# Kernel optimization log

Hardware: AMD Instinct MI355X
Metric: run time of the kernel (lower is better)

Reference implementation:

```python
import jax, jax.numpy as jnp
from jax import lax
import numpy as np

B, T, C = 4, 2048, 1024
H = 4                      # num_heads
D = C // H                 # head_dim
EPS_N = 1e-6               # normalizer eps in scan
EPS_GN = 1e-5              # GroupNorm eps (torch default)


def setup_inputs() -> dict:
    key = jax.random.key(0)
    ks = jax.random.split(key, 8)
    s = 0.02
    return {
        "x": jax.random.normal(ks[0], (B, T, C), jnp.float32),
        "conv_w": jax.random.normal(ks[1], (C, 1, 4), jnp.float32) * s,
        "conv_b": jax.random.normal(ks[2], (C,), jnp.float32) * s,
        "wx_w": jax.random.normal(ks[3], (4 * C, C), jnp.float32) * s,
        "wx_b": jax.random.normal(ks[4], (4 * C,), jnp.float32) * s,
        "gn_w": jnp.ones((C,), jnp.float32),
        "gn_b": jnp.zeros((C,), jnp.float32),
        "out_w": jax.random.normal(ks[5], (C, C), jnp.float32) * s,
        "out_b": jax.random.normal(ks[6], (C,), jnp.float32) * s,
    }


def _slstm_scan(i_g, f_g, z_g, o_g):
    # all inputs (B,T,H,D); scan over time
    def step(carry, g):
        c, n, m = carry
        i_t, f_t, z_t, o_t = g
        m_t = jnp.maximum(f_t + m, i_t)
        i_p = jnp.exp(i_t - m_t)
        f_p = jnp.exp(f_t + m - m_t)
        c_t = f_p * c + i_p * z_t
        n_t = f_p * n + i_p
        h_t = jax.nn.sigmoid(o_t) * (c_t / (n_t + EPS_N))
        return (c_t, n_t, m_t), h_t

    tfirst = lambda a: jnp.transpose(a, (1, 0, 2, 3))  # (T,B,H,D)
    init = (jnp.zeros((B, H, D), i_g.dtype),
            jnp.ones((B, H, D), i_g.dtype),
            jnp.zeros((B, H, D), i_g.dtype))
    _, h_seq = lax.scan(step, init, (tfirst(i_g), tfirst(f_g), tfirst(z_g), tfirst(o_g)))
    return jnp.transpose(h_seq, (1, 0, 2, 3))  # (B,T,H,D)


def reference(x, conv_w, conv_b, wx_w, wx_b, gn_w, gn_b, out_w, out_b):
    # causal depthwise conv (torch pad=3 both sides, sliced to first T == left pad 3)
    xc = jnp.transpose(x, (0, 2, 1))  # (B,C,T)
    xc = lax.conv_general_dilated(
        xc, conv_w, window_strides=(1,), padding=[(3, 0)],
        dimension_numbers=("NCH", "OIH", "NCH"), feature_group_count=C)
    xc = jax.nn.silu(xc + conv_b[None, :, None])
    xc = jnp.transpose(xc, (0, 2, 1))  # (B,T,C)

    gates = jnp.einsum("btc,gc->btg", xc, wx_w) + wx_b  # (B,T,4C)
    gates = gates.reshape(B, T, 4, H, D)
    i_g, f_g, z_g, o_g = (gates[:, :, k] for k in range(4))
    z_g = jnp.tanh(z_g)

    h = _slstm_scan(i_g, f_g, z_g, o_g).reshape(B, T, C)

    # GroupNorm(H groups) over (B,C,T): normalize per (batch, group) over (D, T)
    hg = h.reshape(B, T, H, D)
    mean = hg.mean(axis=(1, 3), keepdims=True)
    var = hg.var(axis=(1, 3), keepdims=True)
    hn = ((hg - mean) / jnp.sqrt(var + EPS_GN)).reshape(B, T, C)
    hn = hn * gn_w + gn_b

    out = jnp.einsum("btc,oc->bto", hn, out_w) + out_b
    return out + x  # dropout is identity at inference
```

## Files before the change

### kernel.cpp

```cpp
#include <hip/hip_runtime.h>

#define B_ 4
#define T_ 2048
#define C_ 1024
#define H_ 4
#define D_ 256
#define M_ (B_*T_)
#define N1_ (4*C_)
#define K_ C_
#define LANES_ (B_*C_)
#define CHUNK_ 32
#define NCHUNK_ (T_/CHUNK_)

typedef unsigned short u16;
typedef unsigned int u32;
typedef __bf16 bf16x8 __attribute__((ext_vector_type(8)));
typedef float f32x4 __attribute__((ext_vector_type(4)));
typedef float vf4 __attribute__((ext_vector_type(4)));
typedef unsigned short u16x4 __attribute__((ext_vector_type(4)));
typedef unsigned short u16x8 __attribute__((ext_vector_type(8)));

__device__ __forceinline__ u16 f2bf(float f) {
  union { float f; u32 u; } v; v.f = f;
  u32 u = v.u;
  u32 r = (u + 0x7FFFu + ((u >> 16) & 1u)) >> 16;
  return (u16)r;
}
__device__ __forceinline__ float b2f(u16 h) {
  union { u32 u; float f; } v; v.u = ((u32)h) << 16;
  return v.f;
}

#define NCAST_ ((N1_*K_ + C_*C_) / 2048)

__global__ void prep_kernel(const float* __restrict__ wx_w, const float* __restrict__ out_w,
                            u16* __restrict__ w1p, u16* __restrict__ w2,
                            const float* __restrict__ x, const float* __restrict__ cw,
                            const float* __restrict__ cb, u16* __restrict__ xc,
                            float* __restrict__ stats) {
  if (blockIdx.x < NCAST_) {
    int i8 = (blockIdx.x * 256 + threadIdx.x) * 8;
    u16x8 o;
    if (i8 < N1_ * K_) {
      int n = i8 >> 10, k8 = i8 & 1023;
      const float* src = wx_w + (size_t)(((n & 3) << 10) | (n >> 2)) * K_ + k8;
      vf4 a = *(const vf4*)src;
      vf4 b = *(const vf4*)(src + 4);
#pragma unroll
      for (int j = 0; j < 4; ++j) { o[j] = f2bf(a[j]); o[j + 4] = f2bf(b[j]); }
      *(u16x8*)(w1p + i8) = o;
    } else {
      int j8 = i8 - N1_ * K_;
      vf4 a = *(const vf4*)(out_w + j8);
      vf4 b = *(const vf4*)(out_w + j8 + 4);
#pragma unroll
      for (int j = 0; j < 4; ++j) { o[j] = f2bf(a[j]); o[j + 4] = f2bf(b[j]); }
      *(u16x8*)(w2 + j8) = o;
    }
    return;
  }
  if (blockIdx.x == NCAST_ && threadIdx.x < 32) stats[threadIdx.x] = 0.f;
  int i4 = ((blockIdx.x - NCAST_) * 256 + threadIdx.x) * 4;
  int c = i4 & (C_ - 1);
  int t = (i4 >> 10) & (T_ - 1);
  vf4 acc = *(const vf4*)(cb + c);
  vf4 w0 = *(const vf4*)(cw + (size_t)c * 4);
  vf4 w1 = *(const vf4*)(cw + (size_t)(c + 1) * 4);
  vf4 w2v = *(const vf4*)(cw + (size_t)(c + 2) * 4);
  vf4 w3 = *(const vf4*)(cw + (size_t)(c + 3) * 4);
#pragma unroll
  for (int k = 0; k < 4; ++k) {
    if (t - 3 + k >= 0) {
      vf4 xv = *(const vf4*)(x + (size_t)i4 + (size_t)(k - 3) * C_);
      acc[0] = fmaf(w0[k], xv[0], acc[0]);
      acc[1] = fmaf(w1[k], xv[1], acc[1]);
      acc[2] = fmaf(w2v[k], xv[2], acc[2]);
      acc[3] = fmaf(w3[k], xv[3], acc[3]);
    }
  }
  u16x4 o;
#pragma unroll
  for (int j = 0; j < 4; ++j) {
    float s = acc[j] / (1.f + __expf(-acc[j]));
    o[j] = f2bf(s);
  }
  *(u16x4*)(xc + i4) = o;
}

template <int EPI>
__global__ __launch_bounds__(256, 3)
void gemm_bt(const u16* __restrict__ A, const u16* __restrict__ Bw,
             const float* __restrict__ bias, const float* __restrict__ resid,
             u16* __restrict__ obf, float* __restrict__ of32,
             f32x4* __restrict__ sSum, int M, int N, int K)
{
  __shared__ __align__(16) u16 smem[128 * 136];
  u16* a_s = smem;
  u16* b_s = smem + 128 * 64;

  const int tid  = threadIdx.x;
  const int lane = tid & 63;
  const int l15  = lane & 15;
  const int q    = lane >> 4;
  const int wave = tid >> 6;
  const int wm   = (wave >> 1) * 64;
  const int wn   = (wave & 1) * 64;
  const int bm   = blockIdx.y * 128;
  const int bn   = blockIdx.x * 128;

  const int srow   = wave * 8 + (lane >> 3);
  const int schunk = lane & 7;

  float bias4[4];
#pragma unroll
  for (int sn = 0; sn < 4; ++sn) {
    int gcol = bn + wn + sn * 16 + l15;
    bias4[sn] = (EPI == 0) ? bias[((gcol & 3) << 10) | (gcol >> 2)] : bias[gcol];
  }
  const bool zlane = (EPI == 0) && ((l15 & 3) == 2);

  f32x4 acc[4][4];
#pragma unroll
  for (int i = 0; i < 4; ++i)
#pragma unroll
    for (int j = 0; j < 4; ++j) acc[i][j] = (f32x4){0.f, 0.f, 0.f, 0.f};

  for (int k0 = 0; k0 < K; k0 += 64) {
#pragma unroll
    for (int i = 0; i < 4; ++i) {
      int r = i * 32 + srow;
      int lc = schunk ^ (r & 7);
      const u16* ga = A  + (size_t)(bm + r) * K + k0 + lc * 8;
      const u16* gb = Bw + (size_t)(bn + r) * K + k0 + lc * 8;
      __builtin_amdgcn_global_load_lds(
          (const __attribute__((address_space(1))) u32*)ga,
          (__attribute__((address_space(3))) u32*)&a_s[(i * 32 + wave * 8) * 64],
          16, 0, 0);
      __builtin_amdgcn_global_load_lds(
          (const __attribute__((address_space(1))) u32*)gb,
          (__attribute__((address_space(3))) u32*)&b_s[(i * 32 + wave * 8) * 64],
          16, 0, 0);
    }
    __syncthreads();
#pragma unroll
    for (int kk = 0; kk < 64; kk += 32) {
      const int kc = kk >> 3;
      bf16x8 af[4], bfr[4];
#pragma unroll
      for (int s = 0; s < 4; ++s) {
        int ra = wm + s * 16 + l15;
        int ph = (kc + q) ^ (ra & 7);
        af[s] = *(const bf16x8*)&a_s[ra * 64 + ph * 8];
      }
#pragma unroll
      for (int s = 0; s < 4; ++s) {
        int rb = wn + s * 16 + l15;
        int ph = (kc + q) ^ (rb & 7);
        bfr[s] = *(const bf16x8*)&b_s[rb * 64 + ph * 8];
      }
#pragma unroll
      for (int sm = 0; sm < 4; ++sm)
#pragma unroll
        for (int sn = 0; sn < 4; ++sn)
          acc[sm][sn] = __builtin_amdgcn_mfma_f32_16x16x32_bf16(af[sm], bfr[sn], acc[sm][sn], 0, 0, 0);
    }
    __syncthreads();
  }

  if (EPI == 0) {
#pragma unroll
    for (int smi = 0; smi < 4; ++smi) {
#pragma unroll
      for (int r = 0; r < 4; ++r) {
        int lrow = wm + smi * 16 + q * 4 + r;
#pragma unroll
        for (int sni = 0; sni < 4; ++sni) {
          int lcol = wn + sni * 16 + l15;
          float v = acc[smi][sni][r] + bias4[sni];
          if (zlane) {
            float e = __expf(2.f * v);
            v = (e - 1.f) / (e + 1.f);
          }
          smem[lrow * 136 + lcol] = f2bf(v);
        }
      }
    }
    __syncthreads();
#pragma unroll
    for (int it = 0; it < 8; ++it) {
      int flat = it * 256 + tid;
      int row = flat >> 4;
      int ch  = flat & 15;
      u16x8 vv = *(const u16x8*)&smem[row * 136 + ch * 8];
      *(u16x8*)(obf + (size_t)(bm + row) * N + bn + ch * 8) = vv;
    }
    if (tid < 128) {
      int ch = tid & 31, ck = tid >> 5;
      const u16* sp = smem + (ck * 32) * 136 + ch * 4;
      float F = 0.f, Mx = -1e30f, aBc = 0.f, aBn = 0.f;
#pragma unroll 8
      for (int t = 0; t < CHUNK_; ++t) {
        u16x4 gv = *(const u16x4*)(sp + t * 136);
        float i_t = b2f(gv[0]), f_t = b2f(gv[1]), z_t = b2f(gv[2]);
        float Mf = Mx + f_t;
        float Mn = fmaxf(Mf, i_t);
        float ea = __expf(Mf - Mn), eb = __expf(i_t - Mn);
        aBc = ea * aBc + eb * z_t;
        aBn = ea * aBn + eb;
        F += f_t; Mx = Mn;
      }
      int b = bm >> 11;
      int s = ((bm & 2047) >> 5) + ck;
      int cg = (bn >> 2) + ch;
      sSum[(size_t)s * LANES_ + b * C_ + cg] = (f32x4){F, Mx, aBc, aBn};
    }
  } else {
    float* fs = (float*)smem;
#pragma unroll
    for (int h = 0; h < 2; ++h) {
      __syncthreads();
#pragma unroll
      for (int smi2 = 0; smi2 < 2; ++smi2) {
        int smi = 2 * h + smi2;
#pragma unroll
        for (int r = 0; r < 4; ++r) {
          int slot = (wm >> 1) + smi2 * 16 + q * 4 + r;
#pragma unroll
          for (int sni = 0; sni < 4; ++sni) {
            int lcol = wn + sni * 16 + l15;
            fs[slot * 132 + lcol] = acc[smi][sni][r] + bias4[sni];
          }
        }
      }
      __syncthreads();
#pragma unroll
      for (int it = 0; it < 8; ++it) {
        int flat = it * 256 + tid;
        int slot = flat >> 5;
        int c4 = (flat & 31) * 4;
        int absrow = bm + ((slot & 32) << 1) + (h << 5) + (slot & 31);
        vf4 v = *(const vf4*)&fs[slot * 132 + c4];
        vf4 rv = *(const vf4*)(resid + (size_t)absrow * N + bn + c4);
        v[0] += rv[0]; v[1] += rv[1]; v[2] += rv[2]; v[3] += rv[3];
        *(vf4*)(of32 + (size_t)absrow * N + bn + c4) = v;
      }
    }
  }
}

__global__ void scan_prefix(const f32x4* __restrict__ sSum, f32x4* __restrict__ iSt) {
  int l = blockIdx.x * 256 + threadIdx.x;
  float ct = 0.f, nt = 1.f, mt = 0.f;
#pragma unroll 8
  for (int s = 0; s < NCHUNK_; ++s) {
    int idx = s * LANES_ + l;
    f32x4 S = sSum[idx];
    iSt[idx] = (f32x4){ct, nt, mt, 0.f};
    float mf = mt + S[0];
    float mn = fmaxf(mf, S[1]);
    float a = __expf(mf - mn);
    float bcoef = __expf(S[1] - mn);
    ct = a * ct + bcoef * S[2];
    nt = a * nt + bcoef * S[3];
    mt = mn;
  }
}

__global__ void scan_passB(const u16* __restrict__ gates, const f32x4* __restrict__ iSt,
                           u16* __restrict__ h, float* __restrict__ stats) {
  int tid = blockIdx.x * 256 + threadIdx.x;
  int lp = tid & 2047;
  int s = tid >> 11;
  int b = lp >> 9;
  int c2 = (lp & 511) * 2;
  const u16* g = gates + ((size_t)(b * T_ + s * CHUNK_) * C_ + c2) * 4;
  u16* hp = h + (size_t)(b * T_ + s * CHUNK_) * C_ + c2;
  int idx = s * LANES_ + b * C_ + c2;
  f32x4 S0 = iSt[idx], S1 = iSt[idx + 1];
  float cc0 = S0[0], nn0 = S0[1], mm0 = S0[2];
  float cc1 = S1[0], nn1 = S1[1], mm1 = S1[2];
  float ls = 0.f, lq = 0.f;
#pragma unroll 4
  for (int t = 0; t < CHUNK_; ++t) {
    u16x8 gv = *(const u16x8*)(g + (size_t)t * C_ * 4);
    float h0, h1;
    {
      float i_t = b2f(gv[0]), f_t = b2f(gv[1]), z_t = b2f(gv[2]), o_t = b2f(gv[3]);
      float m_new = fmaxf(f_t + mm0, i_t);
      float i_p = __expf(i_t - m_new);
      float f_p = __expf(f_t + mm0 - m_new);
      cc0 = f_p * cc0 + i_p * z_t;
      nn0 = f_p * nn0 + i_p;
      mm0 = m_new;
      float sig_o = 1.f / (1.f + __expf(-o_t));
      h0 = sig_o * (cc0 / (nn0 + 1e-6f));
    }
    {
      float i_t = b2f(gv[4]), f_t = b2f(gv[5]), z_t = b2f(gv[6]), o_t = b2f(gv[7]);
      float m_new = fmaxf(f_t + mm1, i_t);
      float i_p = __expf(i_t - m_new);
      float f_p = __expf(f_t + mm1 - m_new);
      cc1 = f_p * cc1 + i_p * z_t;
      nn1 = f_p * nn1 + i_p;
      mm1 = m_new;
      float sig_o = 1.f / (1.f + __expf(-o_t));
      h1 = sig_o * (cc1 / (nn1 + 1e-6f));
    }
    u16 hb0 = f2bf(h0), hb1 = f2bf(h1);
    float v0 = b2f(hb0), v1 = b2f(hb1);
    ls += v0 + v1; lq += v0 * v0 + v1 * v1;
    *(u32*)(hp + (size_t)t * C_) = (u32)hb0 | ((u32)hb1 << 16);
  }
  __shared__ float rs[256], rq[256];
  int thr = threadIdx.x;
  rs[thr] = ls; rq[thr] = lq;
  __syncthreads();
  for (int off = 64; off > 0; off >>= 1) {
    if ((thr & 127) < off) { rs[thr] += rs[thr + off]; rq[thr] += rq[thr + off]; }
    __syncthreads();
  }
  if ((thr & 127) == 0) {
    int grp = b * 4 + (c2 >> 8);
    atomicAdd(&stats[grp * 2 + 0], rs[thr]);
    atomicAdd(&stats[grp * 2 + 1], rq[thr]);
  }
}

__global__ void norm_kernel(const u16* __restrict__ h, const float* __restrict__ stats,
                            const float* __restrict__ gn_w, const float* __restrict__ gn_b,
                            u16* __restrict__ hn) {
  int i8 = (blockIdx.x * 256 + threadIdx.x) * 8;
  int c = i8 & (C_ - 1);
  int b = i8 >> 21;
  int grp = b * 4 + (c >> 8);
  const float inv_n = 1.f / (float)(T_ * D_);
  float mean = stats[grp * 2 + 0] * inv_n;
  float var  = stats[grp * 2 + 1] * inv_n - mean * mean;
  float rstd = rsqrtf(var + 1e-5f);
  u16x8 hv = *(const u16x8*)(h + i8);
  vf4 w0 = *(const vf4*)(gn_w + c), w1 = *(const vf4*)(gn_w + c + 4);
  vf4 b0 = *(const vf4*)(gn_b + c), b1 = *(const vf4*)(gn_b + c + 4);
  u16x8 o;
#pragma unroll
  for (int j = 0; j < 4; ++j) {
    o[j]     = f2bf((b2f(hv[j])     - mean) * rstd * w0[j] + b0[j]);
    o[j + 4] = f2bf((b2f(hv[j + 4]) - mean) * rstd * w1[j] + b1[j]);
  }
  *(u16x8*)(hn + i8) = o;
}

extern "C" void kernel_launch(void* const* d_in, const int* in_sizes, int n_in,
                              void* d_out, int out_size, void* d_ws, size_t ws_size,
                              hipStream_t stream) {
  const float* x      = (const float*)d_in[0];
  const float* conv_w = (const float*)d_in[1];
  const float* conv_b = (const float*)d_in[2];
  const float* wx_w   = (const float*)d_in[3];
  const float* wx_b   = (const float*)d_in[4];
  const float* gn_w   = (const float*)d_in[5];
  const float* gn_b   = (const float*)d_in[6];
  const float* out_w  = (const float*)d_in[7];
  const float* out_b  = (const float*)d_in[8];
  float* out = (float*)d_out;

  char* p = (char*)d_ws;
  u16* xc    = (u16*)p; p += (size_t)M_ * K_ * 2;
  u16* w1    = (u16*)p; p += (size_t)N1_ * K_ * 2;
  u16* w2    = (u16*)p; p += (size_t)C_ * C_ * 2;
  u16* gts   = (u16*)p; p += (size_t)M_ * N1_ * 2;
  u16* hb    = (u16*)p; p += (size_t)M_ * C_ * 2;
  u16* hn    = (u16*)p; p += (size_t)M_ * C_ * 2;
  float* stats = (float*)p; p += 256;
  const int nsum = LANES_ * NCHUNK_;
  f32x4* sSum = (f32x4*)p; p += (size_t)nsum * 16;
  f32x4* iSt  = (f32x4*)p; p += (size_t)nsum * 16;

  prep_kernel<<<NCAST_ + (M_ * C_) / 1024, 256, 0, stream>>>(
      wx_w, out_w, w1, w2, x, conv_w, conv_b, xc, stats);

  gemm_bt<0><<<dim3(N1_ / 128, M_ / 128), 256, 0, stream>>>(
      xc, w1, wx_b, nullptr, gts, nullptr, sSum, M_, N1_, K_);

  scan_prefix<<<LANES_ / 256, 256, 0, stream>>>(sSum, iSt);
  scan_passB<<<(2048 * NCHUNK_) / 256, 256, 0, stream>>>(gts, iSt, hb, stats);

  norm_kernel<<<(M_ * C_) / 2048, 256, 0, stream>>>(hb, stats, gn_w, gn_b, hn);

  gemm_bt<1><<<dim3(C_ / 128, M_ / 128), 256, 0, stream>>>(
      hn, w2, out_b, x, nullptr, out, nullptr, M_, C_, K_);
}
```

Baseline: 273.9 us.

## Fuse scan prefix, chunk scan and GroupNorm into one kernel with grid flags

Merges the prefix scan, per-chunk scan and normalization into a single persistent kernel that synchronizes via global atomic flags, keeping h values in registers instead of writing and re-reading an intermediate buffer. Also splits the GEMM epilogue chunk summary across all 256 threads with a two-segment combine. This removes two launches and a full intermediate round-trip but relies on all 512 blocks being co-resident for the spin barrier, and adds register pressure.

```diff
diff --git a/kernel.cpp b/kernel.cpp
--- a/kernel.cpp
+++ b/kernel.cpp
@@ -37,7 +37,7 @@
                             u16* __restrict__ w1p, u16* __restrict__ w2,
                             const float* __restrict__ x, const float* __restrict__ cw,
                             const float* __restrict__ cb, u16* __restrict__ xc,
-                            float* __restrict__ stats) {
+                            float* __restrict__ stats, int* __restrict__ flags) {
   if (blockIdx.x < NCAST_) {
     int i8 = (blockIdx.x * 256 + threadIdx.x) * 8;
     u16x8 o;
@@ -59,7 +59,10 @@
     }
     return;
   }
-  if (blockIdx.x == NCAST_ && threadIdx.x < 32) stats[threadIdx.x] = 0.f;
+  if (blockIdx.x == NCAST_) {
+    if (threadIdx.x < 32) stats[threadIdx.x] = 0.f;
+    else if (threadIdx.x < 48) flags[threadIdx.x - 32] = 0;
+  }
   int i4 = ((blockIdx.x - NCAST_) * 256 + threadIdx.x) * 4;
   int c = i4 & (C_ - 1);
   int t = (i4 >> 10) & (T_ - 1);
@@ -168,6 +171,7 @@
   }
 
   if (EPI == 0) {
+    __shared__ __align__(16) f32x4 seg[256];
 #pragma unroll
     for (int smi = 0; smi < 4; ++smi) {
 #pragma unroll
@@ -194,12 +198,14 @@
       u16x8 vv = *(const u16x8*)&smem[row * 136 + ch * 8];
       *(u16x8*)(obf + (size_t)(bm + row) * N + bn + ch * 8) = vv;
     }
-    if (tid < 128) {
-      int ch = tid & 31, ck = tid >> 5;
-      const u16* sp = smem + (ck * 32) * 136 + ch * 4;
+    {
+      int unit = tid & 127;
+      int half = tid >> 7;
+      int ch = unit & 31, ck = unit >> 5;
+      const u16* sp = smem + (ck * 32 + half * 16) * 136 + ch * 4;
       float F = 0.f, Mx = -1e30f, aBc = 0.f, aBn = 0.f;
-#pragma unroll 8
-      for (int t = 0; t < CHUNK_; ++t) {
+#pragma unroll
+      for (int t = 0; t < 16; ++t) {
         u16x4 gv = *(const u16x4*)(sp + t * 136);
         float i_t = b2f(gv[0]), f_t = b2f(gv[1]), z_t = b2f(gv[2]);
         float Mf = Mx + f_t;
@@ -209,6 +215,17 @@
         aBn = ea * aBn + eb;
         F += f_t; Mx = Mn;
       }
+      seg[tid] = (f32x4){F, Mx, aBc, aBn};
+    }
+    __syncthreads();
+    if (tid < 128) {
+      f32x4 s0 = seg[tid], s1 = seg[tid + 128];
+      float F = s0[0] + s1[0];
+      float Mx = fmaxf(s0[1] + s1[0], s1[1]);
+      float e0 = __expf(s0[1] + s1[0] - Mx), e1 = __expf(s1[1] - Mx);
+      float aBc = e0 * s0[2] + e1 * s1[2];
+      float aBn = e0 * s0[3] + e1 * s1[3];
+      int ch = tid & 31, ck = tid >> 5;
       int b = bm >> 11;
       int s = ((bm & 2047) >> 5) + ck;
       int cg = (bn >> 2) + ch;
@@ -248,39 +265,51 @@
   }
 }
 
-__global__ void scan_prefix(const f32x4* __restrict__ sSum, f32x4* __restrict__ iSt) {
-  int l = blockIdx.x * 256 + threadIdx.x;
-  float ct = 0.f, nt = 1.f, mt = 0.f;
+__global__ void scan_fused(const u16* __restrict__ gates, const f32x4* __restrict__ sSum,
+                           f32x4* __restrict__ iSt, u16* __restrict__ hn,
+                           const float* __restrict__ gn_w, const float* __restrict__ gn_b,
+                           float* __restrict__ stats, int* __restrict__ flags) {
+  const int tid = blockIdx.x * 256 + threadIdx.x;
+  const int thr = threadIdx.x;
+
+  if (blockIdx.x < 16) {
+    int l = tid;
+    float ct = 0.f, nt = 1.f, mt = 0.f;
 #pragma unroll 8
-  for (int s = 0; s < NCHUNK_; ++s) {
-    int idx = s * LANES_ + l;
-    f32x4 S = sSum[idx];
-    iSt[idx] = (f32x4){ct, nt, mt, 0.f};
-    float mf = mt + S[0];
-    float mn = fmaxf(mf, S[1]);
-    float a = __expf(mf - mn);
-    float bcoef = __expf(S[1] - mn);
-    ct = a * ct + bcoef * S[2];
-    nt = a * nt + bcoef * S[3];
-    mt = mn;
-  }
-}
-
-__global__ void scan_passB(const u16* __restrict__ gates, const f32x4* __restrict__ iSt,
-                           u16* __restrict__ h, float* __restrict__ stats) {
-  int tid = blockIdx.x * 256 + threadIdx.x;
-  int lp = tid & 2047;
-  int s = tid >> 11;
-  int b = lp >> 9;
-  int c2 = (lp & 511) * 2;
+    for (int s = 0; s < NCHUNK_; ++s) {
+      int idx = s * LANES_ + l;
+      f32x4 S = sSum[idx];
+      iSt[idx] = (f32x4){ct, nt, mt, 0.f};
+      float mf = mt + S[0];
+      float mn = fmaxf(mf, S[1]);
+      float a = __expf(mf - mn);
+      float bcoef = __expf(S[1] - mn);
+      ct = a * ct + bcoef * S[2];
+      nt = a * nt + bcoef * S[3];
+      mt = mn;
+    }
+    __syncthreads();
+    if (thr == 0)
+      __hip_atomic_fetch_add(&flags[0], 1, __ATOMIC_RELEASE, __HIP_MEMORY_SCOPE_AGENT);
+  }
+  if (thr == 0) {
+    while (__hip_atomic_load(&flags[0], __ATOMIC_ACQUIRE, __HIP_MEMORY_SCOPE_AGENT) < 16)
+      __builtin_amdgcn_s_sleep(4);
+  }
+  __syncthreads();
+
+  const int lp = tid & 2047;
+  const int s = tid >> 11;
+  const int b = lp >> 9;
+  const int c2 = (lp & 511) * 2;
   const u16* g = gates + ((size_t)(b * T_ + s * CHUNK_) * C_ + c2) * 4;
-  u16* hp = h + (size_t)(b * T_ + s * CHUNK_) * C_ + c2;
   int idx = s * LANES_ + b * C_ + c2;
   f32x4 S0 = iSt[idx], S1 = iSt[idx + 1];
   float cc0 = S0[0], nn0 = S0[1], mm0 = S0[2];
   float cc1 = S1[0], nn1 = S1[1], mm1 = S1[2];
   float ls = 0.f, lq = 0.f;
-#pragma unroll 4
+  u32 hreg[CHUNK_];
+#pragma unroll
   for (int t = 0; t < CHUNK_; ++t) {
     u16x8 gv = *(const u16x8*)(g + (size_t)t * C_ * 4);
     float h0, h1;
@@ -309,44 +338,44 @@
     u16 hb0 = f2bf(h0), hb1 = f2bf(h1);
     float v0 = b2f(hb0), v1 = b2f(hb1);
     ls += v0 + v1; lq += v0 * v0 + v1 * v1;
-    *(u32*)(hp + (size_t)t * C_) = (u32)hb0 | ((u32)hb1 << 16);
+    hreg[t] = (u32)hb0 | ((u32)hb1 << 16);
   }
   __shared__ float rs[256], rq[256];
-  int thr = threadIdx.x;
   rs[thr] = ls; rq[thr] = lq;
   __syncthreads();
   for (int off = 64; off > 0; off >>= 1) {
     if ((thr & 127) < off) { rs[thr] += rs[thr + off]; rq[thr] += rq[thr + off]; }
     __syncthreads();
   }
+  const int grp = b * 4 + (c2 >> 8);
   if ((thr & 127) == 0) {
-    int grp = b * 4 + (c2 >> 8);
     atomicAdd(&stats[grp * 2 + 0], rs[thr]);
     atomicAdd(&stats[grp * 2 + 1], rq[thr]);
   }
-}
-
-__global__ void norm_kernel(const u16* __restrict__ h, const float* __restrict__ stats,
-                            const float* __restrict__ gn_w, const float* __restrict__ gn_b,
-                            u16* __restrict__ hn) {
-  int i8 = (blockIdx.x * 256 + threadIdx.x) * 8;
-  int c = i8 & (C_ - 1);
-  int b = i8 >> 21;
-  int grp = b * 4 + (c >> 8);
+  __syncthreads();
+  if (thr == 0)
+    __hip_atomic_fetch_add(&flags[1], 1, __ATOMIC_RELEASE, __HIP_MEMORY_SCOPE_AGENT);
+  if (thr == 0) {
+    while (__hip_atomic_load(&flags[1], __ATOMIC_ACQUIRE, __HIP_MEMORY_SCOPE_AGENT) < 512)
+      __builtin_amdgcn_s_sleep(4);
+  }
+  __syncthreads();
+
   const float inv_n = 1.f / (float)(T_ * D_);
   float mean = stats[grp * 2 + 0] * inv_n;
   float var  = stats[grp * 2 + 1] * inv_n - mean * mean;
   float rstd = rsqrtf(var + 1e-5f);
-  u16x8 hv = *(const u16x8*)(h + i8);
-  vf4 w0 = *(const vf4*)(gn_w + c), w1 = *(const vf4*)(gn_w + c + 4);
-  vf4 b0 = *(const vf4*)(gn_b + c), b1 = *(const vf4*)(gn_b + c + 4);
-  u16x8 o;
-#pragma unroll
-  for (int j = 0; j < 4; ++j) {
-    o[j]     = f2bf((b2f(hv[j])     - mean) * rstd * w0[j] + b0[j]);
-    o[j + 4] = f2bf((b2f(hv[j + 4]) - mean) * rstd * w1[j] + b1[j]);
-  }
-  *(u16x8*)(hn + i8) = o;
+  float w_0 = gn_w[c2], w_1 = gn_w[c2 + 1];
+  float bb0 = gn_b[c2], bb1 = gn_b[c2 + 1];
+  u16* hp = hn + (size_t)(b * T_ + s * CHUNK_) * C_ + c2;
+#pragma unroll
+  for (int t = 0; t < CHUNK_; ++t) {
+    u32 hv = hreg[t];
+    float v0 = b2f((u16)hv), v1 = b2f((u16)(hv >> 16));
+    u16 o0 = f2bf((v0 - mean) * rstd * w_0 + bb0);
+    u16 o1 = f2bf((v1 - mean) * rstd * w_1 + bb1);
+    *(u32*)(hp + (size_t)t * C_) = (u32)o0 | ((u32)o1 << 16);
+  }
 }
 
 extern "C" void kernel_launch(void* const* d_in, const int* in_sizes, int n_in,
@@ -368,23 +397,20 @@
   u16* w1    = (u16*)p; p += (size_t)N1_ * K_ * 2;
   u16* w2    = (u16*)p; p += (size_t)C_ * C_ * 2;
   u16* gts   = (u16*)p; p += (size_t)M_ * N1_ * 2;
-  u16* hb    = (u16*)p; p += (size_t)M_ * C_ * 2;
   u16* hn    = (u16*)p; p += (size_t)M_ * C_ * 2;
   float* stats = (float*)p; p += 256;
+  int* flags = (int*)p; p += 256;
   const int nsum = LANES_ * NCHUNK_;
   f32x4* sSum = (f32x4*)p; p += (size_t)nsum * 16;
   f32x4* iSt  = (f32x4*)p; p += (size_t)nsum * 16;
 
   prep_kernel<<<NCAST_ + (M_ * C_) / 1024, 256, 0, stream>>>(
-      wx_w, out_w, w1, w2, x, conv_w, conv_b, xc, stats);
+      wx_w, out_w, w1, w2, x, conv_w, conv_b, xc, stats, flags);
 
   gemm_bt<0><<<dim3(N1_ / 128, M_ / 128), 256, 0, stream>>>(
       xc, w1, wx_b, nullptr, gts, nullptr, sSum, M_, N1_, K_);
 
-  scan_prefix<<<LANES_ / 256, 256, 0, stream>>>(sSum, iSt);
-  scan_passB<<<(2048 * NCHUNK_) / 256, 256, 0, stream>>>(gts, iSt, hb, stats);
-
-  norm_kernel<<<(M_ * C_) / 2048, 256, 0, stream>>>(hb, stats, gn_w, gn_b, hn);
+  scan_fused<<<512, 256, 0, stream>>>(gts, sSum, iSt, hn, gn_w, gn_b, stats, flags);
 
   gemm_bt<1><<<dim3(C_ / 128, M_ / 128), 256, 0, stream>>>(
       hn, w2, out_b, x, nullptr, out, nullptr, M_, C_, K_);
```

Measured after the change: 381.6 us. +39.3%, slower.

## Fuse chunk-prefix scan into local scan and split GEMM epilogue summary across all threads

Applied to the files above, without the earlier changes.

The separate scan_prefix kernel is removed. Each scan_local thread now recomputes its own incoming state by sequentially combining all preceding chunk summaries, which saves a kernel launch and the iSt round trip through memory at the cost of redundant O(s) work per thread, up to 63 steps for late chunks. In the GEMM epilogue, all 256 threads now compute half-chunk summaries, which are merged through shared memory, instead of only 128 threads each handling a full chunk. This adds a barrier and some extra work that grows unevenly across blocks.

```diff
diff --git a/kernel.cpp b/kernel.cpp
--- a/kernel.cpp
+++ b/kernel.cpp
@@ -168,6 +168,7 @@
   }
 
   if (EPI == 0) {
+    __shared__ __align__(16) f32x4 seg[256];
 #pragma unroll
     for (int smi = 0; smi < 4; ++smi) {
 #pragma unroll
@@ -194,12 +195,14 @@
       u16x8 vv = *(const u16x8*)&smem[row * 136 + ch * 8];
       *(u16x8*)(obf + (size_t)(bm + row) * N + bn + ch * 8) = vv;
     }
-    if (tid < 128) {
-      int ch = tid & 31, ck = tid >> 5;
-      const u16* sp = smem + (ck * 32) * 136 + ch * 4;
+    {
+      int unit = tid & 127;
+      int half = tid >> 7;
+      int ch = unit & 31, ck = unit >> 5;
+      const u16* sp = smem + (ck * 32 + half * 16) * 136 + ch * 4;
       float F = 0.f, Mx = -1e30f, aBc = 0.f, aBn = 0.f;
-#pragma unroll 8
-      for (int t = 0; t < CHUNK_; ++t) {
+#pragma unroll
+      for (int t = 0; t < 16; ++t) {
         u16x4 gv = *(const u16x4*)(sp + t * 136);
         float i_t = b2f(gv[0]), f_t = b2f(gv[1]), z_t = b2f(gv[2]);
         float Mf = Mx + f_t;
@@ -209,6 +212,17 @@
         aBn = ea * aBn + eb;
         F += f_t; Mx = Mn;
       }
+      seg[tid] = (f32x4){F, Mx, aBc, aBn};
+    }
+    __syncthreads();
+    if (tid < 128) {
+      f32x4 s0 = seg[tid], s1 = seg[tid + 128];
+      float F = s0[0] + s1[0];
+      float Mx = fmaxf(s0[1] + s1[0], s1[1]);
+      float e0 = __expf(s0[1] + s1[0] - Mx), e1 = __expf(s1[1] - Mx);
+      float aBc = e0 * s0[2] + e1 * s1[2];
+      float aBn = e0 * s0[3] + e1 * s1[3];
+      int ch = tid & 31, ck = tid >> 5;
       int b = bm >> 11;
       int s = ((bm & 2047) >> 5) + ck;
       int cg = (bn >> 2) + ch;
@@ -248,37 +262,41 @@
   }
 }
 
-__global__ void scan_prefix(const f32x4* __restrict__ sSum, f32x4* __restrict__ iSt) {
-  int l = blockIdx.x * 256 + threadIdx.x;
-  float ct = 0.f, nt = 1.f, mt = 0.f;
-#pragma unroll 8
-  for (int s = 0; s < NCHUNK_; ++s) {
-    int idx = s * LANES_ + l;
-    f32x4 S = sSum[idx];
-    iSt[idx] = (f32x4){ct, nt, mt, 0.f};
-    float mf = mt + S[0];
-    float mn = fmaxf(mf, S[1]);
-    float a = __expf(mf - mn);
-    float bcoef = __expf(S[1] - mn);
-    ct = a * ct + bcoef * S[2];
-    nt = a * nt + bcoef * S[3];
-    mt = mn;
-  }
-}
-
-__global__ void scan_passB(const u16* __restrict__ gates, const f32x4* __restrict__ iSt,
+__global__ void scan_local(const u16* __restrict__ gates, const f32x4* __restrict__ sSum,
                            u16* __restrict__ h, float* __restrict__ stats) {
-  int tid = blockIdx.x * 256 + threadIdx.x;
-  int lp = tid & 2047;
-  int s = tid >> 11;
-  int b = lp >> 9;
-  int c2 = (lp & 511) * 2;
+  const int thr = threadIdx.x;
+  const int tid = blockIdx.x * 256 + thr;
+  const int lp = tid & 2047;
+  const int s = tid >> 11;
+  const int b = lp >> 9;
+  const int c2 = (lp & 511) * 2;
+  const int base = b * C_ + c2;
+
+  float cc0 = 0.f, nn0 = 1.f, mm0 = 0.f;
+  float cc1 = 0.f, nn1 = 1.f, mm1 = 0.f;
+  for (int j = 0; j < s; ++j) {
+    f32x4 S0 = sSum[(size_t)j * LANES_ + base];
+    f32x4 S1 = sSum[(size_t)j * LANES_ + base + 1];
+    {
+      float mf = mm0 + S0[0];
+      float mn = fmaxf(mf, S0[1]);
+      float a = __expf(mf - mn), bc = __expf(S0[1] - mn);
+      cc0 = a * cc0 + bc * S0[2];
+      nn0 = a * nn0 + bc * S0[3];
+      mm0 = mn;
+    }
+    {
+      float mf = mm1 + S1[0];
+      float mn = fmaxf(mf, S1[1]);
+      float a = __expf(mf - mn), bc = __expf(S1[1] - mn);
+      cc1 = a * cc1 + bc * S1[2];
+      nn1 = a * nn1 + bc * S1[3];
+      mm1 = mn;
+    }
+  }
+
   const u16* g = gates + ((size_t)(b * T_ + s * CHUNK_) * C_ + c2) * 4;
   u16* hp = h + (size_t)(b * T_ + s * CHUNK_) * C_ + c2;
-  int idx = s * LANES_ + b * C_ + c2;
-  f32x4 S0 = iSt[idx], S1 = iSt[idx + 1];
-  float cc0 = S0[0], nn0 = S0[1], mm0 = S0[2];
-  float cc1 = S1[0], nn1 = S1[1], mm1 = S1[2];
   float ls = 0.f, lq = 0.f;
 #pragma unroll 4
   for (int t = 0; t < CHUNK_; ++t) {
@@ -312,7 +330,6 @@
     *(u32*)(hp + (size_t)t * C_) = (u32)hb0 | ((u32)hb1 << 16);
   }
   __shared__ float rs[256], rq[256];
-  int thr = threadIdx.x;
   rs[thr] = ls; rq[thr] = lq;
   __syncthreads();
   for (int off = 64; off > 0; off >>= 1) {
@@ -373,7 +390,6 @@
   float* stats = (float*)p; p += 256;
   const int nsum = LANES_ * NCHUNK_;
   f32x4* sSum = (f32x4*)p; p += (size_t)nsum * 16;
-  f32x4* iSt  = (f32x4*)p; p += (size_t)nsum * 16;
 
   prep_kernel<<<NCAST_ + (M_ * C_) / 1024, 256, 0, stream>>>(
       wx_w, out_w, w1, w2, x, conv_w, conv_b, xc, stats);
@@ -381,8 +397,7 @@
   gemm_bt<0><<<dim3(N1_ / 128, M_ / 128), 256, 0, stream>>>(
       xc, w1, wx_b, nullptr, gts, nullptr, sSum, M_, N1_, K_);
 
-  scan_prefix<<<LANES_ / 256, 256, 0, stream>>>(sSum, iSt);
-  scan_passB<<<(2048 * NCHUNK_) / 256, 256, 0, stream>>>(gts, iSt, hb, stats);
+  scan_local<<<512, 256, 0, stream>>>(gts, sSum, hb, stats);
 
   norm_kernel<<<(M_ * C_) / 2048, 256, 0, stream>>>(hb, stats, gn_w, gn_b, hn);
 
```

Result: no change. 277.5 us (+1.3%).
